# Optimization experiments

Hardware: AMD Instinct MI355X
Metric: run time of the kernel (lower is better)

## Reference

```python
import jax, jax.numpy as jnp
import numpy as np

B, L, D, E = 32, 2048, 1024, 2048

def setup_inputs() -> dict:
    key = jax.random.key(0)
    k1, k2, k3, k4, k5 = jax.random.split(key, 5)
    scale_s = 1.0 / np.sqrt(D)
    scale_h = 1.0 / np.sqrt(E)
    return {
        "dec_hidden": jax.random.normal(k1, (B, D), jnp.float32),
        "enc_outputs": jax.random.normal(k2, (B, L, E), jnp.float32),
        "W_s": jax.random.normal(k3, (D, D), jnp.float32) * scale_s,
        "W_h": jax.random.normal(k4, (D, E), jnp.float32) * scale_h,
        "v": jax.random.normal(k5, (D,), jnp.float32) * scale_s,
    }

def reference(dec_hidden, enc_outputs, W_s, W_h, v):
    # s: [B, D] -- projected decoder state (broadcast over src_len, no repeat)
    s = jnp.einsum('bd,ed->be', dec_hidden, W_s)
    # h: [B, L, D] -- projected encoder outputs
    h = jnp.einsum('ble,de->bld', enc_outputs, W_h)
    # additive scores: v^T tanh(s + h) -> [B, L]
    scores = jnp.einsum('bld,d->bl', jnp.tanh(s[:, None, :] + h), v)
    attn = jax.nn.softmax(scores, axis=1)
    # context: weighted sum of encoder outputs -> [B, E]
    ctx = jnp.einsum('bl,ble->be', attn, enc_outputs)
    return (ctx, attn)
```

## Files before the change

kernel.cpp:

```cpp
#include <hip/hip_runtime.h>
#include <cstdint>
#include <cstddef>

#define B_ 32
#define L_ 2048
#define D_ 1024
#define E_ 2048

typedef __attribute__((ext_vector_type(8))) short short8;
typedef __attribute__((ext_vector_type(16))) float f32x16;
typedef __attribute__((ext_vector_type(4))) unsigned int uint4v;

__device__ __forceinline__ void async_copy16(const void* g, void* l) {
  __builtin_amdgcn_global_load_lds((const __attribute__((address_space(1))) void*)g,
                                   (__attribute__((address_space(3))) void*)l, 16, 0, 0);
}

__device__ __forceinline__ unsigned int pack_bf16_2(float lo, float hi) {
  unsigned int ul = __builtin_bit_cast(unsigned int, lo) + 0x8000u;
  unsigned int uh = __builtin_bit_cast(unsigned int, hi) + 0x8000u;
  return (ul >> 16) | (uh & 0xFFFF0000u);
}

__device__ __forceinline__ float fast_tanh(float x) {
  float e = __expf(2.0f * x);
  return 1.0f - 2.0f / (e + 1.0f);
}

__global__ __launch_bounds__(256) void k_s(const float* __restrict__ dec,
                                           const float* __restrict__ Ws,
                                           float* __restrict__ s) {
  int wid = threadIdx.x >> 6, lane = threadIdx.x & 63;
  int out = blockIdx.x * 4 + wid;
  int b = out >> 10, i = out & 1023;
  const float* dr = dec + b * D_;
  const float* wr = Ws + (size_t)i * D_;
  float acc = 0.f;
#pragma unroll
  for (int c = 0; c < 4; ++c) {
    int d0 = c * 256 + lane * 4;
    float4 x = *(const float4*)(dr + d0);
    float4 w = *(const float4*)(wr + d0);
    acc += x.x * w.x + x.y * w.y + x.z * w.z + x.w * w.w;
  }
#pragma unroll
  for (int off = 32; off >= 1; off >>= 1) acc += __shfl_xor(acc, off, 64);
  if (lane == 0) s[out] = acc;
}

__global__ __launch_bounds__(256) void k_cvt(const float* __restrict__ src,
                                             unsigned short* __restrict__ dst) {
  size_t i = ((size_t)blockIdx.x * 256 + threadIdx.x) * 8;
  float4 a = *(const float4*)(src + i);
  float4 b = *(const float4*)(src + i + 4);
  uint4v p;
  p.x = pack_bf16_2(a.x, a.y);
  p.y = pack_bf16_2(a.z, a.w);
  p.z = pack_bf16_2(b.x, b.y);
  p.w = pack_bf16_2(b.z, b.w);
  *(uint4v*)(dst + i) = p;
}

__global__ __launch_bounds__(128, 2) void k_gemm(const float* __restrict__ enc,
                                                 const unsigned short* __restrict__ whb,
                                                 const float* __restrict__ sbias,
                                                 const float* __restrict__ vvec,
                                                 float* __restrict__ scores) {
  __shared__ alignas(16) float As[128 * 32];
  __shared__ alignas(16) unsigned short Bs[128 * 32];

  const int tid = threadIdx.x;
  const int wid = tid >> 6;
  const int lane = tid & 63;

  const int flat = blockIdx.x;
  const int nt = (flat >> 3) & 7;
  const int mt = (flat & 7) | ((flat >> 6) << 3);
  const int m_base = mt * 128, n_base = nt * 128;
  const int b_idx = m_base >> 11;

  const int aRowL = lane >> 3;
  const int aColF = ((lane & 7) ^ (aRowL & 7)) * 4;
  const float* gA = enc + (size_t)(m_base + wid * 64 + aRowL) * E_ + aColF;
  {
  }
  const int bUnit = (lane & 7) ^ ((lane >> 3) & 7);
  const int bRow0 = 2 * (lane >> 3) + (bUnit >> 2);
  const int bKoff = (bUnit & 3) * 8;
  const unsigned short* gB = whb + (size_t)(n_base + wid * 64 + bRow0) * E_ + bKoff;

  const int col = lane & 31;
  const int h = lane >> 5;
  const unsigned short* bptr[4][2];
#pragma unroll
  for (int ni = 0; ni < 4; ++ni)
#pragma unroll
    for (int ks = 0; ks < 2; ++ks) {
      int line = ni * 16 + (col >> 1);
      int unit = (col & 1) * 4 + ks * 2 + h;
      bptr[ni][ks] = &Bs[line * 64 + ((unit ^ (line & 7)) * 8)];
    }
  const float* aptr[2][2][2];
#pragma unroll
  for (int mi = 0; mi < 2; ++mi)
#pragma unroll
    for (int ks = 0; ks < 2; ++ks)
#pragma unroll
      for (int j = 0; j < 2; ++j) {
        int r = wid * 64 + mi * 32 + col;
        int u = ks * 4 + h * 2 + j;
        aptr[mi][ks][j] = &As[r * 32 + ((u ^ (r & 7)) * 4)];
      }

  f32x16 acc[2][4] = {};

  for (int kk = 0; kk < E_; kk += 32) {
    __syncthreads();
#pragma unroll
    for (int it = 0; it < 8; ++it)
      async_copy16(gA + (size_t)(it * 8) * E_ + kk, &As[(wid * 64 + it * 8) * 32]);
#pragma unroll
    for (int it = 0; it < 4; ++it)
      async_copy16(gB + (size_t)(it * 16) * E_ + kk, &Bs[(wid * 64 + it * 16) * 32]);
    __syncthreads();

#pragma unroll
    for (int ks = 0; ks < 2; ++ks) {
      short8 bf[4];
#pragma unroll
      for (int ni = 0; ni < 4; ++ni) bf[ni] = *(const short8*)bptr[ni][ks];
#pragma unroll
      for (int mi = 0; mi < 2; ++mi) {
        float4 f0 = *(const float4*)aptr[mi][ks][0];
        float4 f1 = *(const float4*)aptr[mi][ks][1];
        uint4v pa;
        pa.x = pack_bf16_2(f0.x, f0.y);
        pa.y = pack_bf16_2(f0.z, f0.w);
        pa.z = pack_bf16_2(f1.x, f1.y);
        pa.w = pack_bf16_2(f1.z, f1.w);
        short8 af = __builtin_bit_cast(short8, pa);
#pragma unroll
        for (int ni = 0; ni < 4; ++ni)
          acc[mi][ni] = __builtin_amdgcn_mfma_f32_32x32x16_bf16(af, bf[ni], acc[mi][ni], 0, 0, 0);
      }
    }
  }

  float vv[4], sv[4];
#pragma unroll
  for (int ni = 0; ni < 4; ++ni) {
    int n = n_base + ni * 32 + col;
    vv[ni] = vvec[n];
    sv[ni] = sbias[b_idx * D_ + n];
  }
#pragma unroll
  for (int mi = 0; mi < 2; ++mi) {
#pragma unroll
    for (int reg = 0; reg < 16; ++reg) {
      float sum = 0.f;
#pragma unroll
      for (int ni = 0; ni < 4; ++ni)
        sum += vv[ni] * fast_tanh(sv[ni] + acc[mi][ni][reg]);
      sum += __shfl_xor(sum, 1, 64);
      sum += __shfl_xor(sum, 2, 64);
      sum += __shfl_xor(sum, 4, 64);
      sum += __shfl_xor(sum, 8, 64);
      sum += __shfl_xor(sum, 16, 64);
      if (col == 0)
        atomicAdd(&scores[m_base + wid * 64 + mi * 32 + (reg & 3) + 8 * (reg >> 2) + h * 4], sum);
    }
  }
}

__global__ __launch_bounds__(256) void k_softmax(float* __restrict__ sc) {
  int b = blockIdx.x, tid = threadIdx.x;
  int lane = tid & 63, wid = tid >> 6;
  float* row = sc + (size_t)b * L_;
  float vals[8];
  float mx = -1e30f;
#pragma unroll
  for (int j = 0; j < 8; ++j) { vals[j] = row[tid + j * 256]; mx = fmaxf(mx, vals[j]); }
#pragma unroll
  for (int off = 32; off >= 1; off >>= 1) mx = fmaxf(mx, __shfl_xor(mx, off, 64));
  __shared__ float redm[4], reds[4];
  if (lane == 0) redm[wid] = mx;
  __syncthreads();
  mx = fmaxf(fmaxf(redm[0], redm[1]), fmaxf(redm[2], redm[3]));
  float sum = 0.f;
#pragma unroll
  for (int j = 0; j < 8; ++j) { vals[j] = __expf(vals[j] - mx); sum += vals[j]; }
#pragma unroll
  for (int off = 32; off >= 1; off >>= 1) sum += __shfl_xor(sum, off, 64);
  if (lane == 0) reds[wid] = sum;
  __syncthreads();
  sum = reds[0] + reds[1] + reds[2] + reds[3];
  float inv = 1.0f / sum;
#pragma unroll
  for (int j = 0; j < 8; ++j) row[tid + j * 256] = vals[j] * inv;
}

__global__ __launch_bounds__(256) void k_ctx(const float* __restrict__ enc,
                                             const float* __restrict__ attn,
                                             float* __restrict__ ctx) {
  int b = blockIdx.y, lc = blockIdx.x;
  int t = threadIdx.x;
  __shared__ float aw[128];
  if (t < 128) aw[t] = attn[(size_t)b * L_ + lc * 128 + t];
  __syncthreads();
  const float* base = enc + ((size_t)b * L_ + (size_t)lc * 128) * E_;
  float4 a0 = make_float4(0.f, 0.f, 0.f, 0.f);
  float4 a1 = make_float4(0.f, 0.f, 0.f, 0.f);
#pragma unroll 2
  for (int l = 0; l < 128; ++l) {
    float w = aw[l];
    const float* r = base + (size_t)l * E_;
    float4 x0 = *(const float4*)(r + t * 4);
    float4 x1 = *(const float4*)(r + 1024 + t * 4);
    a0.x += w * x0.x; a0.y += w * x0.y; a0.z += w * x0.z; a0.w += w * x0.w;
    a1.x += w * x1.x; a1.y += w * x1.y; a1.z += w * x1.z; a1.w += w * x1.w;
  }
  float* cb = ctx + (size_t)b * E_;
  atomicAdd(cb + t * 4 + 0, a0.x);
  atomicAdd(cb + t * 4 + 1, a0.y);
  atomicAdd(cb + t * 4 + 2, a0.z);
  atomicAdd(cb + t * 4 + 3, a0.w);
  atomicAdd(cb + 1024 + t * 4 + 0, a1.x);
  atomicAdd(cb + 1024 + t * 4 + 1, a1.y);
  atomicAdd(cb + 1024 + t * 4 + 2, a1.z);
  atomicAdd(cb + 1024 + t * 4 + 3, a1.w);
}

extern "C" void kernel_launch(void* const* d_in, const int* in_sizes, int n_in,
                              void* d_out, int out_size, void* d_ws, size_t ws_size,
                              hipStream_t stream) {
  const float* dec = (const float*)d_in[0];
  const float* enc = (const float*)d_in[1];
  const float* Ws  = (const float*)d_in[2];
  const float* Wh  = (const float*)d_in[3];
  const float* v   = (const float*)d_in[4];

  float* ctx  = (float*)d_out;
  float* attn = (float*)d_out + B_ * E_;

  unsigned short* whb = (unsigned short*)d_ws;
  float* sbuf = (float*)((char*)d_ws + (size_t)D_ * E_ * sizeof(unsigned short));

  hipMemsetAsync(d_out, 0, (size_t)out_size * sizeof(float), stream);

  k_s<<<dim3((B_ * D_) / 4), dim3(256), 0, stream>>>(dec, Ws, sbuf);
  k_cvt<<<dim3((D_ * E_) / (256 * 8)), dim3(256), 0, stream>>>(Wh, whb);
  k_gemm<<<dim3((B_ * L_ / 128) * (D_ / 128)), dim3(128), 0, stream>>>(enc, whb, sbuf, v, attn);
  k_softmax<<<dim3(B_), dim3(256), 0, stream>>>(attn);
  k_ctx<<<dim3(L_ / 128, B_), dim3(256), 0, stream>>>(enc, attn, ctx);
}
```

Measured before the change: 1.147 ms.

## Restructure GEMM to 4 waves with 2x2 warp tiling and K=64 stages; split ctx

The scores GEMM moves from 2 waves each computing 64x128 to 4 waves in a 2x2 layout, each computing 64x64. The K step per LDS stage doubles to 64, which halves the number of barrier pairs, and the LDS swizzle and load offsets are redone for the wider tiles. Launch bounds become 256 threads with 3 blocks per CU, trading fewer accumulators per wave for more waves in flight to hide latency. The context kernel is also split into finer blocks (64 rows by half of E), giving more parallelism at the cost of more atomic adds.

Result: faster. 1.111 ms (-3.2%).

```diff
diff --git a/kernel.cpp b/kernel.cpp
--- a/kernel.cpp
+++ b/kernel.cpp
@@ -61,17 +61,19 @@
   *(uint4v*)(dst + i) = p;
 }
 
-__global__ __launch_bounds__(128, 2) void k_gemm(const float* __restrict__ enc,
+__global__ __launch_bounds__(256, 3) void k_gemm(const float* __restrict__ enc,
                                                  const unsigned short* __restrict__ whb,
                                                  const float* __restrict__ sbias,
                                                  const float* __restrict__ vvec,
                                                  float* __restrict__ scores) {
-  __shared__ alignas(16) float As[128 * 32];
-  __shared__ alignas(16) unsigned short Bs[128 * 32];
+  __shared__ alignas(16) float As[128 * 64];
+  __shared__ alignas(16) unsigned short Bs[64 * 128];
 
   const int tid = threadIdx.x;
   const int wid = tid >> 6;
   const int lane = tid & 63;
+  const int wm = wid >> 1;
+  const int wn = wid & 1;
 
   const int flat = blockIdx.x;
   const int nt = (flat >> 3) & 7;
@@ -79,60 +81,62 @@
   const int m_base = mt * 128, n_base = nt * 128;
   const int b_idx = m_base >> 11;
 
-  const int aRowL = lane >> 3;
-  const int aColF = ((lane & 7) ^ (aRowL & 7)) * 4;
-  const float* gA = enc + (size_t)(m_base + wid * 64 + aRowL) * E_ + aColF;
-  {
-  }
-  const int bUnit = (lane & 7) ^ ((lane >> 3) & 7);
-  const int bRow0 = 2 * (lane >> 3) + (bUnit >> 2);
-  const int bKoff = (bUnit & 3) * 8;
-  const unsigned short* gB = whb + (size_t)(n_base + wid * 64 + bRow0) * E_ + bKoff;
+  const int rp = lane >> 4;
+  const int ul = lane & 15;
+  const int u0 = ul ^ rp;
+  const float* gA = enc + (size_t)(m_base + wid * 32 + rp) * E_;
+  int offA[8];
+#pragma unroll
+  for (int it = 0; it < 8; ++it)
+    offA[it] = it * 4 * E_ + ((u0 ^ ((it & 3) << 2)) << 2);
+  const unsigned short* gB = whb + (size_t)n_base * E_;
+  int offB[4];
+#pragma unroll
+  for (int it = 0; it < 4; ++it) {
+    int ulog = u0 ^ (it << 2);
+    offB[it] = (wid * 32 + it * 8 + 2 * rp + (ulog >> 3)) * E_ + (ulog & 7) * 8;
+  }
 
   const int col = lane & 31;
   const int h = lane >> 5;
-  const unsigned short* bptr[4][2];
-#pragma unroll
-  for (int ni = 0; ni < 4; ++ni)
-#pragma unroll
-    for (int ks = 0; ks < 2; ++ks) {
-      int line = ni * 16 + (col >> 1);
-      int unit = (col & 1) * 4 + ks * 2 + h;
-      bptr[ni][ks] = &Bs[line * 64 + ((unit ^ (line & 7)) * 8)];
-    }
-  const float* aptr[2][2][2];
-#pragma unroll
-  for (int mi = 0; mi < 2; ++mi)
-#pragma unroll
-    for (int ks = 0; ks < 2; ++ks)
-#pragma unroll
-      for (int j = 0; j < 2; ++j) {
-        int r = wid * 64 + mi * 32 + col;
-        int u = ks * 4 + h * 2 + j;
-        aptr[mi][ks][j] = &As[r * 32 + ((u ^ (r & 7)) * 4)];
-      }
-
-  f32x16 acc[2][4] = {};
-
-  for (int kk = 0; kk < E_; kk += 32) {
+  const float* arow[2];
+#pragma unroll
+  for (int mi = 0; mi < 2; ++mi) arow[mi] = &As[(wm * 64 + mi * 32 + col) * 64];
+  int aoff[4][2];
+#pragma unroll
+  for (int ks = 0; ks < 4; ++ks)
+#pragma unroll
+    for (int j = 0; j < 2; ++j)
+      aoff[ks][j] = ((ks * 4 + h * 2 + j) ^ (col & 15)) * 4;
+  const unsigned short* brow[2];
+#pragma unroll
+  for (int ni = 0; ni < 2; ++ni) brow[ni] = &Bs[(wn * 32 + ni * 16 + (col >> 1)) * 128];
+  int boff[4];
+#pragma unroll
+  for (int ks = 0; ks < 4; ++ks)
+    boff[ks] = ((((col & 1) << 3) + ks * 2 + h) ^ ((col >> 1) & 15)) * 8;
+
+  f32x16 acc[2][2] = {};
+
+  for (int kk = 0; kk < E_; kk += 64) {
     __syncthreads();
 #pragma unroll
     for (int it = 0; it < 8; ++it)
-      async_copy16(gA + (size_t)(it * 8) * E_ + kk, &As[(wid * 64 + it * 8) * 32]);
+      async_copy16(gA + offA[it] + kk, &As[(wid * 32 + it * 4) * 64]);
 #pragma unroll
     for (int it = 0; it < 4; ++it)
-      async_copy16(gB + (size_t)(it * 16) * E_ + kk, &Bs[(wid * 64 + it * 16) * 32]);
+      async_copy16(gB + offB[it] + kk, &Bs[(wid * 16 + it * 4) * 128]);
     __syncthreads();
 
 #pragma unroll
-    for (int ks = 0; ks < 2; ++ks) {
-      short8 bf[4];
-#pragma unroll
-      for (int ni = 0; ni < 4; ++ni) bf[ni] = *(const short8*)bptr[ni][ks];
+    for (int ks = 0; ks < 4; ++ks) {
+      short8 bf[2];
+#pragma unroll
+      for (int ni = 0; ni < 2; ++ni) bf[ni] = *(const short8*)(brow[ni] + boff[ks]);
 #pragma unroll
       for (int mi = 0; mi < 2; ++mi) {
-        float4 f0 = *(const float4*)aptr[mi][ks][0];
-        float4 f1 = *(const float4*)aptr[mi][ks][1];
+        float4 f0 = *(const float4*)(arow[mi] + aoff[ks][0]);
+        float4 f1 = *(const float4*)(arow[mi] + aoff[ks][1]);
         uint4v pa;
         pa.x = pack_bf16_2(f0.x, f0.y);
         pa.y = pack_bf16_2(f0.z, f0.w);
@@ -140,16 +144,16 @@
         pa.w = pack_bf16_2(f1.z, f1.w);
         short8 af = __builtin_bit_cast(short8, pa);
 #pragma unroll
-        for (int ni = 0; ni < 4; ++ni)
+        for (int ni = 0; ni < 2; ++ni)
           acc[mi][ni] = __builtin_amdgcn_mfma_f32_32x32x16_bf16(af, bf[ni], acc[mi][ni], 0, 0, 0);
       }
     }
   }
 
-  float vv[4], sv[4];
-#pragma unroll
-  for (int ni = 0; ni < 4; ++ni) {
-    int n = n_base + ni * 32 + col;
+  float vv[2], sv[2];
+#pragma unroll
+  for (int ni = 0; ni < 2; ++ni) {
+    int n = n_base + wn * 64 + ni * 32 + col;
     vv[ni] = vvec[n];
     sv[ni] = sbias[b_idx * D_ + n];
   }
@@ -159,7 +163,7 @@
     for (int reg = 0; reg < 16; ++reg) {
       float sum = 0.f;
 #pragma unroll
-      for (int ni = 0; ni < 4; ++ni)
+      for (int ni = 0; ni < 2; ++ni)
         sum += vv[ni] * fast_tanh(sv[ni] + acc[mi][ni][reg]);
       sum += __shfl_xor(sum, 1, 64);
       sum += __shfl_xor(sum, 2, 64);
@@ -167,7 +171,7 @@
       sum += __shfl_xor(sum, 8, 64);
       sum += __shfl_xor(sum, 16, 64);
       if (col == 0)
-        atomicAdd(&scores[m_base + wid * 64 + mi * 32 + (reg & 3) + 8 * (reg >> 2) + h * 4], sum);
+        atomicAdd(&scores[m_base + wm * 64 + mi * 32 + (reg & 3) + 8 * (reg >> 2) + h * 4], sum);
     }
   }
 }
@@ -202,32 +206,26 @@
 __global__ __launch_bounds__(256) void k_ctx(const float* __restrict__ enc,
                                              const float* __restrict__ attn,
                                              float* __restrict__ ctx) {
-  int b = blockIdx.y, lc = blockIdx.x;
+  int b = blockIdx.y;
+  int lc = blockIdx.x >> 1;
+  int eh = blockIdx.x & 1;
   int t = threadIdx.x;
-  __shared__ float aw[128];
-  if (t < 128) aw[t] = attn[(size_t)b * L_ + lc * 128 + t];
+  __shared__ float aw[64];
+  if (t < 64) aw[t] = attn[(size_t)b * L_ + lc * 64 + t];
   __syncthreads();
-  const float* base = enc + ((size_t)b * L_ + (size_t)lc * 128) * E_;
+  const float* base = enc + ((size_t)b * L_ + (size_t)lc * 64) * E_ + eh * 1024;
   float4 a0 = make_float4(0.f, 0.f, 0.f, 0.f);
-  float4 a1 = make_float4(0.f, 0.f, 0.f, 0.f);
-#pragma unroll 2
-  for (int l = 0; l < 128; ++l) {
+#pragma unroll 4
+  for (int l = 0; l < 64; ++l) {
     float w = aw[l];
-    const float* r = base + (size_t)l * E_;
-    float4 x0 = *(const float4*)(r + t * 4);
-    float4 x1 = *(const float4*)(r + 1024 + t * 4);
+    float4 x0 = *(const float4*)(base + (size_t)l * E_ + t * 4);
     a0.x += w * x0.x; a0.y += w * x0.y; a0.z += w * x0.z; a0.w += w * x0.w;
-    a1.x += w * x1.x; a1.y += w * x1.y; a1.z += w * x1.z; a1.w += w * x1.w;
-  }
-  float* cb = ctx + (size_t)b * E_;
-  atomicAdd(cb + t * 4 + 0, a0.x);
-  atomicAdd(cb + t * 4 + 1, a0.y);
-  atomicAdd(cb + t * 4 + 2, a0.z);
-  atomicAdd(cb + t * 4 + 3, a0.w);
-  atomicAdd(cb + 1024 + t * 4 + 0, a1.x);
-  atomicAdd(cb + 1024 + t * 4 + 1, a1.y);
-  atomicAdd(cb + 1024 + t * 4 + 2, a1.z);
-  atomicAdd(cb + 1024 + t * 4 + 3, a1.w);
+  }
+  float* cb = ctx + (size_t)b * E_ + eh * 1024 + t * 4;
+  atomicAdd(cb + 0, a0.x);
+  atomicAdd(cb + 1, a0.y);
+  atomicAdd(cb + 2, a0.z);
+  atomicAdd(cb + 3, a0.w);
 }
 
 extern "C" void kernel_launch(void* const* d_in, const int* in_sizes, int n_in,
@@ -249,7 +247,7 @@
 
   k_s<<<dim3((B_ * D_) / 4), dim3(256), 0, stream>>>(dec, Ws, sbuf);
   k_cvt<<<dim3((D_ * E_) / (256 * 8)), dim3(256), 0, stream>>>(Wh, whb);
-  k_gemm<<<dim3((B_ * L_ / 128) * (D_ / 128)), dim3(128), 0, stream>>>(enc, whb, sbuf, v, attn);
+  k_gemm<<<dim3((B_ * L_ / 128) * (D_ / 128)), dim3(256), 0, stream>>>(enc, whb, sbuf, v, attn);
   k_softmax<<<dim3(B_), dim3(256), 0, stream>>>(attn);
-  k_ctx<<<dim3(L_ / 128, B_), dim3(256), 0, stream>>>(enc, attn, ctx);
-}
+  k_ctx<<<dim3(64, B_), dim3(256), 0, stream>>>(enc, attn, ctx);
+}
```
